# Kernel optimization log

Measured on AMD Instinct MI355X. Metric: run time of the kernel, lower is better.

The kernel has to match this reference:

```python
import jax, jax.numpy as jnp
from jax import lax
import numpy as np

D_MODEL = 1024
D_STATE = 16
D_CONV = 4
EXPAND = 2
D_INNER = EXPAND * D_MODEL
BATCH = 2
SEQLEN = 1024


def setup_inputs() -> dict:
    key = jax.random.key(0)
    ks = jax.random.split(key, 8)
    x = jax.random.normal(ks[0], (BATCH, SEQLEN, D_MODEL), jnp.float32)
    W_in = jax.random.normal(ks[1], (2 * D_INNER, D_MODEL), jnp.float32) * (1.0 / np.sqrt(D_MODEL))
    conv_w = jax.random.normal(ks[2], (D_INNER, 1, D_CONV), jnp.float32) * (1.0 / np.sqrt(D_CONV))
    conv_b = jax.random.normal(ks[3], (D_INNER,), jnp.float32) * 0.02
    W_x = jax.random.normal(ks[4], (2 * D_STATE, D_INNER), jnp.float32) * (1.0 / np.sqrt(D_INNER))
    W_dt = jax.random.normal(ks[5], (D_INNER, D_INNER), jnp.float32) * (1.0 / np.sqrt(D_INNER))
    b_dt = jax.random.normal(ks[6], (D_INNER,), jnp.float32) * 0.02
    # A_log = log(arange(1..d_state)) repeated over d_inner rows, as in __init__
    A_log = jnp.log(jnp.tile(jnp.arange(1, D_STATE + 1, dtype=jnp.float32), (D_INNER, 1)))
    D = jnp.ones((D_INNER,), jnp.float32)
    W_out = jax.random.normal(ks[7], (D_MODEL, D_INNER), jnp.float32) * (1.0 / np.sqrt(D_INNER))
    return {"x": x, "W_in": W_in, "conv_w": conv_w, "conv_b": conv_b,
            "W_x": W_x, "W_dt": W_dt, "b_dt": b_dt, "A_log": A_log,
            "D": D, "W_out": W_out}


def reference(x, W_in, conv_w, conv_b, W_x, W_dt, b_dt, A_log, D, W_out):
    d_inner, _, d_conv = conv_w.shape
    d_state = A_log.shape[1]

    # in_proj and split into x / gate z
    xz = x @ W_in.T                                   # (B, L, 2*d_inner)
    xi, z = jnp.split(xz, 2, axis=-1)

    # causal depthwise conv1d: torch pads both sides by d_conv-1 then slices
    # [:seqlen], which equals left-only padding of d_conv-1
    xc = lax.conv_general_dilated(
        xi.transpose(0, 2, 1), conv_w, window_strides=(1,),
        padding=[(d_conv - 1, 0)],
        dimension_numbers=("NCH", "OIH", "NCH"),
        feature_group_count=d_inner)
    xc = xc + conv_b[None, :, None]
    u = jax.nn.silu(xc.transpose(0, 2, 1))            # (B, L, d_inner)

    # input-dependent B, C and dt
    BC = u @ W_x.T                                    # (B, L, 2*d_state)
    Bmat, Cmat = jnp.split(BC, 2, axis=-1)
    dt = jax.nn.softplus(u @ W_dt.T + b_dt)           # (B, L, d_inner)

    A = -jnp.exp(A_log)                               # (d_inner, d_state)
    dA = jnp.exp(dt[..., None] * A)                   # (B, L, d_inner, d_state)
    dBu = dt[..., None] * Bmat[:, :, None, :] * u[..., None]

    def step(s, inp):
        dA_t, dBu_t, C_t = inp
        s = dA_t * s + dBu_t                          # (B, d_inner, d_state)
        y_t = jnp.einsum("bdn,bn->bd", s, C_t)
        return s, y_t

    s0 = jnp.zeros((x.shape[0], d_inner, d_state), x.dtype)
    _, ys = lax.scan(step, s0,
                     (dA.transpose(1, 0, 2, 3),
                      dBu.transpose(1, 0, 2, 3),
                      Cmat.transpose(1, 0, 2)))
    y = ys.transpose(1, 0, 2) + D * u                 # (B, L, d_inner)

    y = y * jax.nn.silu(z)
    # dropout is identity in eval mode
    return y @ W_out.T
```

## Files before the change

kernel.cpp:

```cpp
#include <hip/hip_runtime.h>
#include <hip/hip_bf16.h>
#include <math.h>

#define B_SZ   2
#define LSEQ   1024
#define DMODEL 1024
#define DSTATE 16
#define DCONV  4
#define DINNER 2048
#define MROWS  (B_SZ * LSEQ)
#define NCHUNK 32
#define TCHUNK (LSEQ / NCHUNK)
#define NCAT   2176
#define BKS    64

typedef __attribute__((ext_vector_type(8))) short bf16x8;
typedef __attribute__((ext_vector_type(4))) float f32x4;

__device__ __forceinline__ void gl2lds16(const void* g, void* l) {
    __builtin_amdgcn_global_load_lds(
        (const __attribute__((address_space(1))) void*)g,
        (__attribute__((address_space(3))) void*)l, 16, 0, 0);
}

__global__ __launch_bounds__(256)
void cvt_bf16(const float* __restrict__ in, __hip_bfloat16* __restrict__ out)
{
    int i = (blockIdx.x * 256 + threadIdx.x) * 8;
    float4 a = *(const float4*)&in[i];
    float4 b = *(const float4*)&in[i + 4];
    union { __hip_bfloat16 h[8]; int4 v; } o;
    o.h[0] = __float2bfloat16(a.x); o.h[1] = __float2bfloat16(a.y);
    o.h[2] = __float2bfloat16(a.z); o.h[3] = __float2bfloat16(a.w);
    o.h[4] = __float2bfloat16(b.x); o.h[5] = __float2bfloat16(b.y);
    o.h[6] = __float2bfloat16(b.z); o.h[7] = __float2bfloat16(b.w);
    *(int4*)&out[i] = o.v;
}

template<int EPI>
__global__ __launch_bounds__(256)
void gemm_bt(const __hip_bfloat16* __restrict__ A,
             const __hip_bfloat16* __restrict__ B,
             const float* __restrict__ bias,
             float* __restrict__ Cbase, size_t pstride, int ldc,
             float* __restrict__ C2,
             int K, int klen)
{
    constexpr int BN   = 64;
    constexpr int NLD  = (128 + BN) / 8 / 4;
    constexpr int SMEL = (128 + BN) * BKS;
    __shared__ __hip_bfloat16 sm[2 * SMEL];

    const int tid  = threadIdx.x;
    const int lane = tid & 63;
    const int w    = tid >> 6;
    const int m0 = blockIdx.x * 128;
    const int n0 = blockIdx.y * BN;
    const int wr = w >> 1, wc = w & 1;
    const int kbase = blockIdx.z * klen;
    float* __restrict__ C = Cbase + (size_t)blockIdx.z * pstride;

    const int lrow = lane >> 3;
    const int swc  = ((lane & 7) ^ lrow) * 8;
    const __hip_bfloat16* srcp[NLD];
    #pragma unroll
    for (int i = 0; i < NLD; ++i) {
        const int q = w + 4 * i;
        srcp[i] = (q < 16)
            ? A + (size_t)(m0 + q * 8 + lrow) * K + kbase + swc
            : B + (size_t)(n0 + (q - 16) * 8 + lrow) * K + kbase + swc;
    }

    f32x4 acc[4][2] = {};
    const int l7 = lane & 7, l15 = lane & 15, lq = lane >> 4;
    const int sw0 = (lq ^ l7) * 8;
    const int sw1 = sw0 ^ 32;

    #pragma unroll
    for (int i = 0; i < NLD; ++i)
        gl2lds16(srcp[i], sm + (w + 4 * i) * 512);
    asm volatile("s_waitcnt vmcnt(0)" ::: "memory");
    __builtin_amdgcn_s_barrier();
    __builtin_amdgcn_sched_barrier(0);

    const int nt = klen / BKS;
    int buf = 0;
    for (int t = 0; t < nt; ++t) {
        if (t + 1 < nt) {
            #pragma unroll
            for (int i = 0; i < NLD; ++i)
                gl2lds16(srcp[i] + (size_t)(t + 1) * BKS,
                         sm + (buf ^ 1) * SMEL + (w + 4 * i) * 512);
        }
        const __hip_bfloat16* As = sm + buf * SMEL;
        const __hip_bfloat16* Bs = As + 128 * BKS;
        bf16x8 a0[4], a1[4], b0[2], b1[2];
        #pragma unroll
        for (int m = 0; m < 4; ++m) {
            const int r = (wr * 64 + m * 16 + l15) * BKS;
            a0[m] = *(const bf16x8*)&As[r + sw0];
            a1[m] = *(const bf16x8*)&As[r + sw1];
        }
        #pragma unroll
        for (int n = 0; n < 2; ++n) {
            const int r = (wc * 32 + n * 16 + l15) * BKS;
            b0[n] = *(const bf16x8*)&Bs[r + sw0];
            b1[n] = *(const bf16x8*)&Bs[r + sw1];
        }
        #pragma unroll
        for (int m = 0; m < 4; ++m)
            #pragma unroll
            for (int n = 0; n < 2; ++n) {
                acc[m][n] = __builtin_amdgcn_mfma_f32_16x16x32_bf16(
                    a0[m], b0[n], acc[m][n], 0, 0, 0);
                acc[m][n] = __builtin_amdgcn_mfma_f32_16x16x32_bf16(
                    a1[m], b1[n], acc[m][n], 0, 0, 0);
            }
        asm volatile("s_waitcnt vmcnt(0)" ::: "memory");
        __builtin_amdgcn_s_barrier();
        __builtin_amdgcn_sched_barrier(0);
        buf ^= 1;
    }

    #pragma unroll
    for (int m = 0; m < 4; ++m)
        #pragma unroll
        for (int n = 0; n < 2; ++n) {
            const int col = n0 + wc * 32 + n * 16 + l15;
            #pragma unroll
            for (int j = 0; j < 4; ++j) {
                const int row = m0 + wr * 64 + m * 16 + lq * 4 + j;
                float v = acc[m][n][j];
                if (EPI == 0) {
                    C[(size_t)row * ldc + col] = v;
                } else {
                    if (col < DINNER) {
                        v += bias[col];
                        v = (v > 20.f) ? v : log1pf(__expf(v));
                        C[(size_t)row * ldc + col] = v;
                    } else if (col < DINNER + 32) {
                        C2[(size_t)row * 32 + (col - DINNER)] = v;
                    }
                }
            }
        }
}

__global__ __launch_bounds__(256)
void add4(const float* __restrict__ p, float* __restrict__ o)
{
    const size_t S = (size_t)MROWS * DMODEL;
    int i = (blockIdx.x * 256 + threadIdx.x) * 4;
    float4 a = *(const float4*)&p[i];
    float4 b = *(const float4*)&p[i + S];
    float4 c = *(const float4*)&p[i + 2 * S];
    float4 d = *(const float4*)&p[i + 3 * S];
    a.x += b.x + c.x + d.x; a.y += b.y + c.y + d.y;
    a.z += b.z + c.z + d.z; a.w += b.w + c.w + d.w;
    *(float4*)&o[i] = a;
}

__global__ __launch_bounds__(256)
void conv_silu(const float* __restrict__ xz, const float* __restrict__ cw,
               const float* __restrict__ cb, float* __restrict__ u,
               __hip_bfloat16* __restrict__ u_bf)
{
    int idx = blockIdx.x * blockDim.x + threadIdx.x;
    int d = idx & (DINNER - 1);
    int m = idx >> 11;
    int t = m & (LSEQ - 1);
    float acc = cb[d];
    #pragma unroll
    for (int j = 0; j < DCONV; ++j) {
        int tt = t - (DCONV - 1) + j;
        if (tt >= 0)
            acc += xz[(size_t)(m - t + tt) * 4096 + d] * cw[d * DCONV + j];
    }
    float v = acc / (1.f + __expf(-acc));
    u[(size_t)m * DINNER + d] = v;
    u_bf[(size_t)m * DINNER + d] = __float2bfloat16(v);
}

__global__ __launch_bounds__(256)
void scan_part1(const float* __restrict__ dt, const float* __restrict__ u,
                const float* __restrict__ bc, const float* __restrict__ A_log,
                float* __restrict__ s_end, float* __restrict__ dtsum)
{
    const int d = blockIdx.x * 256 + threadIdx.x;
    const int c = blockIdx.y;
    const int b = blockIdx.z;
    __shared__ float bcs[TCHUNK][32];
    {
        int f = threadIdx.x * 4;
        const float* src = bc + ((size_t)b * LSEQ + c * TCHUNK) * 32;
        *(float4*)&bcs[f >> 5][f & 31] = *(const float4*)&src[f];
    }
    float An[16];
    {
        float4 a0 = *(const float4*)&A_log[d * DSTATE + 0];
        float4 a1 = *(const float4*)&A_log[d * DSTATE + 4];
        float4 a2 = *(const float4*)&A_log[d * DSTATE + 8];
        float4 a3 = *(const float4*)&A_log[d * DSTATE + 12];
        An[0]=-__expf(a0.x); An[1]=-__expf(a0.y); An[2]=-__expf(a0.z); An[3]=-__expf(a0.w);
        An[4]=-__expf(a1.x); An[5]=-__expf(a1.y); An[6]=-__expf(a1.z); An[7]=-__expf(a1.w);
        An[8]=-__expf(a2.x); An[9]=-__expf(a2.y); An[10]=-__expf(a2.z); An[11]=-__expf(a2.w);
        An[12]=-__expf(a3.x); An[13]=-__expf(a3.y); An[14]=-__expf(a3.z); An[15]=-__expf(a3.w);
    }
    __syncthreads();
    const float* dtp = dt + ((size_t)b * LSEQ + c * TCHUNK) * DINNER + d;
    const float* up  = u  + ((size_t)b * LSEQ + c * TCHUNK) * DINNER + d;
    float s[16] = {};
    float sum = 0.f;
    for (int t = 0; t < TCHUNK; ++t) {
        float dtv = dtp[(size_t)t * DINNER];
        float uv  = up [(size_t)t * DINNER];
        sum += dtv;
        float du = dtv * uv;
        #pragma unroll
        for (int n = 0; n < 16; ++n) {
            float a = __expf(dtv * An[n]);
            s[n] = a * s[n] + du * bcs[t][n];
        }
    }
    float* se = s_end + ((size_t)(b * NCHUNK + c) * DINNER + d) * 16;
    #pragma unroll
    for (int q = 0; q < 4; ++q)
        *(float4*)&se[q * 4] = make_float4(s[q*4], s[q*4+1], s[q*4+2], s[q*4+3]);
    dtsum[(size_t)(b * NCHUNK + c) * DINNER + d] = sum;
}

__global__ __launch_bounds__(256)
void scan_combine(float* __restrict__ s_end, const float* __restrict__ dtsum,
                  const float* __restrict__ A_log)
{
    int idx = blockIdx.x * 256 + threadIdx.x;
    int n = idx & 15;
    int d = (idx >> 4) & (DINNER - 1);
    int b = idx >> 15;
    float An = -__expf(A_log[d * DSTATE + n]);
    float s = 0.f;
    for (int c = 0; c < NCHUNK; ++c) {
        size_t base = (size_t)(b * NCHUNK + c) * DINNER + d;
        float se = s_end[base * 16 + n];
        s_end[base * 16 + n] = s;
        float P = __expf(An * dtsum[base]);
        s = P * s + se;
    }
}

__global__ __launch_bounds__(256)
void scan_part2(const float* __restrict__ dt, const float* __restrict__ u,
                const float* __restrict__ bc, const float* __restrict__ s_in,
                const float* __restrict__ A_log, const float* __restrict__ Dp,
                const float* __restrict__ xz, __hip_bfloat16* __restrict__ y_bf)
{
    const int d = blockIdx.x * 256 + threadIdx.x;
    const int c = blockIdx.y;
    const int b = blockIdx.z;
    __shared__ float bcs[TCHUNK][32];
    {
        int f = threadIdx.x * 4;
        const float* src = bc + ((size_t)b * LSEQ + c * TCHUNK) * 32;
        *(float4*)&bcs[f >> 5][f & 31] = *(const float4*)&src[f];
    }
    float An[16];
    {
        float4 a0 = *(const float4*)&A_log[d * DSTATE + 0];
        float4 a1 = *(const float4*)&A_log[d * DSTATE + 4];
        float4 a2 = *(const float4*)&A_log[d * DSTATE + 8];
        float4 a3 = *(const float4*)&A_log[d * DSTATE + 12];
        An[0]=-__expf(a0.x); An[1]=-__expf(a0.y); An[2]=-__expf(a0.z); An[3]=-__expf(a0.w);
        An[4]=-__expf(a1.x); An[5]=-__expf(a1.y); An[6]=-__expf(a1.z); An[7]=-__expf(a1.w);
        An[8]=-__expf(a2.x); An[9]=-__expf(a2.y); An[10]=-__expf(a2.z); An[11]=-__expf(a2.w);
        An[12]=-__expf(a3.x); An[13]=-__expf(a3.y); An[14]=-__expf(a3.z); An[15]=-__expf(a3.w);
    }
    float s[16];
    {
        const float* si = s_in + ((size_t)(b * NCHUNK + c) * DINNER + d) * 16;
        #pragma unroll
        for (int q = 0; q < 4; ++q) {
            float4 v = *(const float4*)&si[q * 4];
            s[q*4] = v.x; s[q*4+1] = v.y; s[q*4+2] = v.z; s[q*4+3] = v.w;
        }
    }
    const float Dd = Dp[d];
    __syncthreads();
    const float* dtp = dt + ((size_t)b * LSEQ + c * TCHUNK) * DINNER + d;
    const float* up  = u  + ((size_t)b * LSEQ + c * TCHUNK) * DINNER + d;
    const float* zp  = xz + ((size_t)b * LSEQ + c * TCHUNK) * 4096 + 2048 + d;
    __hip_bfloat16* yp = y_bf + ((size_t)b * LSEQ + c * TCHUNK) * DINNER + d;
    for (int t = 0; t < TCHUNK; ++t) {
        float dtv = dtp[(size_t)t * DINNER];
        float uv  = up [(size_t)t * DINNER];
        float du = dtv * uv;
        float y = Dd * uv;
        #pragma unroll
        for (int n = 0; n < 16; ++n) {
            float a = __expf(dtv * An[n]);
            s[n] = a * s[n] + du * bcs[t][n];
            y += s[n] * bcs[t][16 + n];
        }
        float zv = zp[(size_t)t * 4096];
        yp[(size_t)t * DINNER] = __float2bfloat16(y * (zv / (1.f + __expf(-zv))));
    }
}

extern "C" void kernel_launch(void* const* d_in, const int* in_sizes, int n_in,
                              void* d_out, int out_size, void* d_ws, size_t ws_size,
                              hipStream_t stream)
{
    const float* x      = (const float*)d_in[0];
    const float* W_in   = (const float*)d_in[1];
    const float* conv_w = (const float*)d_in[2];
    const float* conv_b = (const float*)d_in[3];
    const float* W_x    = (const float*)d_in[4];
    const float* W_dt   = (const float*)d_in[5];
    const float* b_dt   = (const float*)d_in[6];
    const float* A_log  = (const float*)d_in[7];
    const float* Dp     = (const float*)d_in[8];
    const float* W_out  = (const float*)d_in[9];
    float* out = (float*)d_out;

    const size_t MB = 1ull << 20;
    char* w8 = (char*)d_ws;
    float* xz    = (float*)(w8);
    float* p3    = (float*)(w8);
    float* u     = (float*)(w8 + 32*MB);
    float* dtc   = (float*)(w8 + 48*MB);
    float* bc    = (float*)(w8 + 64*MB);
    float* sbuf  = (float*)(w8 + 65*MB);
    float* dtsum = (float*)(w8 + 73*MB);
    __hip_bfloat16* u_bf   = (__hip_bfloat16*)(w8 + 74*MB);
    __hip_bfloat16* x_bf   = (__hip_bfloat16*)(w8 + 82*MB);
    __hip_bfloat16* Win_bf = (__hip_bfloat16*)(w8 + 86*MB);
    __hip_bfloat16* Wcat_bf= (__hip_bfloat16*)(w8 + 82*MB);
    __hip_bfloat16* Wout_bf= (__hip_bfloat16*)(w8 + 90*MB + 512*1024);
    __hip_bfloat16* y_bf   = (__hip_bfloat16*)(w8 + 82*MB);
    Wout_bf = (__hip_bfloat16*)(w8 + 90*MB);

    cvt_bf16<<<(MROWS * DMODEL) / 2048, 256, 0, stream>>>(x, x_bf);
    cvt_bf16<<<(4096 * DMODEL) / 2048, 256, 0, stream>>>(W_in, Win_bf);
    gemm_bt<0><<<dim3(16, 64, 1), 256, 0, stream>>>(
        x_bf, Win_bf, nullptr, xz, 0, 4096, nullptr, DMODEL, DMODEL);
    conv_silu<<<(MROWS * DINNER) / 256, 256, 0, stream>>>(xz, conv_w, conv_b, u, u_bf);
    cvt_bf16<<<(DINNER * DINNER) / 2048, 256, 0, stream>>>(W_dt, Wcat_bf);
    cvt_bf16<<<(32 * DINNER) / 2048, 256, 0, stream>>>(W_x, Wcat_bf + (size_t)DINNER * DINNER);
    gemm_bt<2><<<dim3(16, NCAT / 64, 1), 256, 0, stream>>>(
        u_bf, Wcat_bf, b_dt, dtc, 0, DINNER, bc, DINNER, DINNER);
    cvt_bf16<<<(DMODEL * DINNER) / 2048, 256, 0, stream>>>(W_out, Wout_bf);
    scan_part1<<<dim3(DINNER/256, NCHUNK, B_SZ), 256, 0, stream>>>(
        dtc, u, bc, A_log, sbuf, dtsum);
    scan_combine<<<(B_SZ * DINNER * DSTATE) / 256, 256, 0, stream>>>(
        sbuf, dtsum, A_log);
    scan_part2<<<dim3(DINNER/256, NCHUNK, B_SZ), 256, 0, stream>>>(
        dtc, u, bc, sbuf, A_log, Dp, xz, y_bf);
    gemm_bt<0><<<dim3(16, 16, 4), 256, 0, stream>>>(
        y_bf, Wout_bf, nullptr, p3, (size_t)MROWS * DMODEL, DMODEL, nullptr,
        DINNER, DINNER / 4);
    add4<<<(MROWS * DMODEL) / 1024, 256, 0, stream>>>(p3, out);
}
```

Baseline: 194.4 us.

## Load GEMM B operand directly into registers and merge bf16 conversion launches

The GEMM no longer stages the B tile through LDS. Each wave loads its B fragments straight from global memory into registers and double-buffers them across an unrolled pair of k-steps, which halves LDS footprint and LDS read traffic for B. The cost is uncoalesced per-lane global reads of B that are repeated by the two wave rows, plus the loop now assumes an even number of k tiles. Separately, pairs of fp32-to-bf16 conversion kernels are merged into one launch to cut launch overhead.

Result: slower. 246.8 us (+26.9%).

```diff
diff --git a/kernel.cpp b/kernel.cpp
--- a/kernel.cpp
+++ b/kernel.cpp
@@ -23,10 +23,9 @@
         (__attribute__((address_space(3))) void*)l, 16, 0, 0);
 }
 
-__global__ __launch_bounds__(256)
-void cvt_bf16(const float* __restrict__ in, __hip_bfloat16* __restrict__ out)
-{
-    int i = (blockIdx.x * 256 + threadIdx.x) * 8;
+__device__ __forceinline__ void cvt8(const float* __restrict__ in,
+                                     __hip_bfloat16* __restrict__ out, int i)
+{
     float4 a = *(const float4*)&in[i];
     float4 b = *(const float4*)&in[i + 4];
     union { __hip_bfloat16 h[8]; int4 v; } o;
@@ -37,6 +36,22 @@
     *(int4*)&out[i] = o.v;
 }
 
+__global__ __launch_bounds__(256)
+void cvt_bf16(const float* __restrict__ in, __hip_bfloat16* __restrict__ out)
+{
+    cvt8(in, out, (blockIdx.x * 256 + threadIdx.x) * 8);
+}
+
+__global__ __launch_bounds__(256)
+void cvt_bf16_2(const float* __restrict__ s0, __hip_bfloat16* __restrict__ d0,
+                int nb0,
+                const float* __restrict__ s1, __hip_bfloat16* __restrict__ d1)
+{
+    const int b = blockIdx.x;
+    if (b < nb0) cvt8(s0, d0, b * 2048 + threadIdx.x * 8);
+    else         cvt8(s1, d1, (b - nb0) * 2048 + threadIdx.x * 8);
+}
+
 template<int EPI>
 __global__ __launch_bounds__(256)
 void gemm_bt(const __hip_bfloat16* __restrict__ A,
@@ -46,81 +61,92 @@
              float* __restrict__ C2,
              int K, int klen)
 {
-    constexpr int BN   = 64;
-    constexpr int NLD  = (128 + BN) / 8 / 4;
-    constexpr int SMEL = (128 + BN) * BKS;
+    constexpr int SMEL = 128 * BKS;
     __shared__ __hip_bfloat16 sm[2 * SMEL];
 
     const int tid  = threadIdx.x;
     const int lane = tid & 63;
     const int w    = tid >> 6;
     const int m0 = blockIdx.x * 128;
-    const int n0 = blockIdx.y * BN;
+    const int n0 = blockIdx.y * 64;
     const int wr = w >> 1, wc = w & 1;
     const int kbase = blockIdx.z * klen;
     float* __restrict__ C = Cbase + (size_t)blockIdx.z * pstride;
 
     const int lrow = lane >> 3;
-    const int swc  = ((lane & 7) ^ lrow) * 8;
-    const __hip_bfloat16* srcp[NLD];
-    #pragma unroll
-    for (int i = 0; i < NLD; ++i) {
+    const int swcol = ((lane & 7) ^ lrow) * 8;
+    const __hip_bfloat16* srcp[4];
+    #pragma unroll
+    for (int i = 0; i < 4; ++i) {
         const int q = w + 4 * i;
-        srcp[i] = (q < 16)
-            ? A + (size_t)(m0 + q * 8 + lrow) * K + kbase + swc
-            : B + (size_t)(n0 + (q - 16) * 8 + lrow) * K + kbase + swc;
-    }
-
-    f32x4 acc[4][2] = {};
+        srcp[i] = A + (size_t)(m0 + q * 8 + lrow) * K + kbase + swcol;
+    }
+
     const int l7 = lane & 7, l15 = lane & 15, lq = lane >> 4;
     const int sw0 = (lq ^ l7) * 8;
     const int sw1 = sw0 ^ 32;
 
-    #pragma unroll
-    for (int i = 0; i < NLD; ++i)
+    const __hip_bfloat16* Bp0 = B + (size_t)(n0 + wc * 32 + l15) * K + kbase + lq * 8;
+    const __hip_bfloat16* Bp1 = Bp0 + (size_t)16 * K;
+
+    f32x4 acc[4][2] = {};
+    const int nt = klen / BKS;
+
+    bf16x8 bA[4], bB[4];
+    #pragma unroll
+    for (int i = 0; i < 4; ++i)
         gl2lds16(srcp[i], sm + (w + 4 * i) * 512);
+    bA[0] = *(const bf16x8*)(Bp0);
+    bA[1] = *(const bf16x8*)(Bp0 + 32);
+    bA[2] = *(const bf16x8*)(Bp1);
+    bA[3] = *(const bf16x8*)(Bp1 + 32);
     asm volatile("s_waitcnt vmcnt(0)" ::: "memory");
     __builtin_amdgcn_s_barrier();
     __builtin_amdgcn_sched_barrier(0);
 
-    const int nt = klen / BKS;
     int buf = 0;
-    for (int t = 0; t < nt; ++t) {
-        if (t + 1 < nt) {
-            #pragma unroll
-            for (int i = 0; i < NLD; ++i)
-                gl2lds16(srcp[i] + (size_t)(t + 1) * BKS,
-                         sm + (buf ^ 1) * SMEL + (w + 4 * i) * 512);
-        }
-        const __hip_bfloat16* As = sm + buf * SMEL;
-        const __hip_bfloat16* Bs = As + 128 * BKS;
-        bf16x8 a0[4], a1[4], b0[2], b1[2];
-        #pragma unroll
-        for (int m = 0; m < 4; ++m) {
-            const int r = (wr * 64 + m * 16 + l15) * BKS;
-            a0[m] = *(const bf16x8*)&As[r + sw0];
-            a1[m] = *(const bf16x8*)&As[r + sw1];
-        }
-        #pragma unroll
-        for (int n = 0; n < 2; ++n) {
-            const int r = (wc * 32 + n * 16 + l15) * BKS;
-            b0[n] = *(const bf16x8*)&Bs[r + sw0];
-            b1[n] = *(const bf16x8*)&Bs[r + sw1];
-        }
-        #pragma unroll
-        for (int m = 0; m < 4; ++m)
-            #pragma unroll
-            for (int n = 0; n < 2; ++n) {
-                acc[m][n] = __builtin_amdgcn_mfma_f32_16x16x32_bf16(
-                    a0[m], b0[n], acc[m][n], 0, 0, 0);
-                acc[m][n] = __builtin_amdgcn_mfma_f32_16x16x32_bf16(
-                    a1[m], b1[n], acc[m][n], 0, 0, 0);
-            }
-        asm volatile("s_waitcnt vmcnt(0)" ::: "memory");
-        __builtin_amdgcn_s_barrier();
-        __builtin_amdgcn_sched_barrier(0);
-        buf ^= 1;
-    }
+    #define GEMM_STEP(T, BCUR, BNXT)                                          \
+    {                                                                         \
+        const int t_ = (T);                                                   \
+        if (t_ + 1 < nt) {                                                    \
+            _Pragma("unroll")                                                 \
+            for (int i = 0; i < 4; ++i)                                       \
+                gl2lds16(srcp[i] + (size_t)(t_ + 1) * BKS,                    \
+                         sm + (buf ^ 1) * SMEL + (w + 4 * i) * 512);          \
+        }                                                                     \
+        const size_t ko_ = (size_t)((t_ + 1 < nt) ? t_ + 1 : t_) * BKS;       \
+        BNXT[0] = *(const bf16x8*)(Bp0 + ko_);                                \
+        BNXT[1] = *(const bf16x8*)(Bp0 + ko_ + 32);                           \
+        BNXT[2] = *(const bf16x8*)(Bp1 + ko_);                                \
+        BNXT[3] = *(const bf16x8*)(Bp1 + ko_ + 32);                           \
+        const __hip_bfloat16* As_ = sm + buf * SMEL;                          \
+        bf16x8 a0_[4], a1_[4];                                                \
+        _Pragma("unroll")                                                     \
+        for (int m = 0; m < 4; ++m) {                                         \
+            const int r_ = (wr * 64 + m * 16 + l15) * BKS;                    \
+            a0_[m] = *(const bf16x8*)&As_[r_ + sw0];                          \
+            a1_[m] = *(const bf16x8*)&As_[r_ + sw1];                          \
+        }                                                                     \
+        _Pragma("unroll")                                                     \
+        for (int m = 0; m < 4; ++m)                                           \
+            _Pragma("unroll")                                                 \
+            for (int n = 0; n < 2; ++n) {                                     \
+                acc[m][n] = __builtin_amdgcn_mfma_f32_16x16x32_bf16(          \
+                    a0_[m], BCUR[2 * n], acc[m][n], 0, 0, 0);                 \
+                acc[m][n] = __builtin_amdgcn_mfma_f32_16x16x32_bf16(          \
+                    a1_[m], BCUR[2 * n + 1], acc[m][n], 0, 0, 0);             \
+            }                                                                 \
+        asm volatile("s_waitcnt vmcnt(0)" ::: "memory");                      \
+        __builtin_amdgcn_s_barrier();                                         \
+        __builtin_amdgcn_sched_barrier(0);                                    \
+        buf ^= 1;                                                             \
+    }
+
+    for (int tt = 0; tt < nt; tt += 2) {
+        GEMM_STEP(tt,     bA, bB);
+        GEMM_STEP(tt + 1, bB, bA);
+    }
+    #undef GEMM_STEP
 
     #pragma unroll
     for (int m = 0; m < 4; ++m)
@@ -334,17 +360,15 @@
     __hip_bfloat16* x_bf   = (__hip_bfloat16*)(w8 + 82*MB);
     __hip_bfloat16* Win_bf = (__hip_bfloat16*)(w8 + 86*MB);
     __hip_bfloat16* Wcat_bf= (__hip_bfloat16*)(w8 + 82*MB);
-    __hip_bfloat16* Wout_bf= (__hip_bfloat16*)(w8 + 90*MB + 512*1024);
     __hip_bfloat16* y_bf   = (__hip_bfloat16*)(w8 + 82*MB);
-    Wout_bf = (__hip_bfloat16*)(w8 + 90*MB);
-
-    cvt_bf16<<<(MROWS * DMODEL) / 2048, 256, 0, stream>>>(x, x_bf);
-    cvt_bf16<<<(4096 * DMODEL) / 2048, 256, 0, stream>>>(W_in, Win_bf);
+    __hip_bfloat16* Wout_bf= (__hip_bfloat16*)(w8 + 90*MB);
+
+    cvt_bf16_2<<<1024 + 2048, 256, 0, stream>>>(x, x_bf, 1024, W_in, Win_bf);
     gemm_bt<0><<<dim3(16, 64, 1), 256, 0, stream>>>(
         x_bf, Win_bf, nullptr, xz, 0, 4096, nullptr, DMODEL, DMODEL);
     conv_silu<<<(MROWS * DINNER) / 256, 256, 0, stream>>>(xz, conv_w, conv_b, u, u_bf);
-    cvt_bf16<<<(DINNER * DINNER) / 2048, 256, 0, stream>>>(W_dt, Wcat_bf);
-    cvt_bf16<<<(32 * DINNER) / 2048, 256, 0, stream>>>(W_x, Wcat_bf + (size_t)DINNER * DINNER);
+    cvt_bf16_2<<<2048 + 32, 256, 0, stream>>>(W_dt, Wcat_bf, 2048,
+                                              W_x, Wcat_bf + (size_t)DINNER * DINNER);
     gemm_bt<2><<<dim3(16, NCAT / 64, 1), 256, 0, stream>>>(
         u_bf, Wcat_bf, b_dt, dtc, 0, DINNER, bc, DINNER, DINNER);
     cvt_bf16<<<(DMODEL * DINNER) / 2048, 256, 0, stream>>>(W_out, Wout_bf);
```
